# Optimization experiments

Hardware: AMD Instinct MI355X
Metric: run time of the kernel (lower is better)

## Reference

```python
import jax, jax.numpy as jnp
import numpy as np

SHIFT = 1
EPS = 1e-5

def setup_inputs() -> dict:
    key = jax.random.key(0)
    k1, k2, k3, k4, k5, k6 = jax.random.split(key, 6)
    B, C, H, Wd = 64, 512, 28, 28
    Cout = 512
    return {
        "x": jax.random.normal(k1, (B, C, H, Wd), dtype=jnp.float32),
        "W": jax.random.normal(k2, (Cout, C), dtype=jnp.float32) * 0.05,
        "gamma": jax.random.uniform(k3, (Cout,), dtype=jnp.float32) + 0.5,
        "beta": jax.random.normal(k4, (Cout,), dtype=jnp.float32) * 0.1,
        "running_mean": jax.random.normal(k5, (Cout,), dtype=jnp.float32) * 0.1,
        "running_var": jax.random.uniform(k6, (Cout,), dtype=jnp.float32) + 0.5,
    }

def reference(x, W, gamma, beta, running_mean, running_var):
    # Group-wise spatial shift: split channels into 4 groups, roll each.
    Cg = x.shape[1] // 4
    x1 = jnp.roll(x[:, 0*Cg:1*Cg], -SHIFT, axis=2)  # up
    x2 = jnp.roll(x[:, 1*Cg:2*Cg],  SHIFT, axis=2)  # down
    x3 = jnp.roll(x[:, 2*Cg:3*Cg], -SHIFT, axis=3)  # left
    x4 = jnp.roll(x[:, 3*Cg:4*Cg],  SHIFT, axis=3)  # right
    shifted = jnp.concatenate([x1, x2, x3, x4], axis=1)  # [B,C,H,W]
    # 1x1 conv (no bias) == channel matmul
    y = jnp.einsum('bchw,oc->bohw', shifted, W)
    # BatchNorm (inference: running stats) folded to scale/shift, then ReLU
    scale = gamma * jax.lax.rsqrt(running_var + EPS)
    shift = beta - running_mean * scale
    y = y * scale[None, :, None, None] + shift[None, :, None, None]
    return jnp.maximum(y, 0.0)
```

## Files before the change

kernel.cpp:

```cpp
#include <hip/hip_runtime.h>
#include <hip/hip_bf16.h>

#define BN   64
#define CIN  512
#define COUT 512
#define HW   784
#define NT   128
#define MT   112
#define BK   64
#define SW_STRIDE 72
#define SX_STRIDE 64

typedef __attribute__((ext_vector_type(8))) short short8;
typedef __attribute__((ext_vector_type(4))) float f32x4;

__device__ __forceinline__ unsigned short f2bf(float f) {
    union { float f; unsigned int u; } v; v.f = f;
    unsigned int r = v.u + 0x7fffu + ((v.u >> 16) & 1u);
    return (unsigned short)(r >> 16);
}

__device__ __forceinline__ uint2 pack4(float a, float b, float c, float d) {
    uint2 r;
    r.x = (unsigned int)f2bf(a) | ((unsigned int)f2bf(b) << 16);
    r.y = (unsigned int)f2bf(c) | ((unsigned int)f2bf(d) << 16);
    return r;
}

__global__ void wconv_kernel(const float* __restrict__ W, unsigned short* __restrict__ Wb) {
    int i = (blockIdx.x * 256 + threadIdx.x) * 8;
    float4 a = *(const float4*)(W + i);
    float4 b = *(const float4*)(W + i + 4);
    uint2 lo = pack4(a.x, a.y, a.z, a.w);
    uint2 hi = pack4(b.x, b.y, b.z, b.w);
    uint4 v; v.x = lo.x; v.y = lo.y; v.z = hi.x; v.w = hi.y;
    *(uint4*)(Wb + i) = v;
}

template<bool PREW>
__global__ __launch_bounds__(256, 2)
void shiftconv_kernel(const float* __restrict__ x,
                      const void* __restrict__ Wp,
                      const float* __restrict__ gamma,
                      const float* __restrict__ beta,
                      const float* __restrict__ rmean,
                      const float* __restrict__ rvar,
                      float* __restrict__ out)
{
    __shared__ unsigned short sW[NT * SW_STRIDE];
    __shared__ unsigned short sX[MT * SX_STRIDE];

    const int t = threadIdx.x;
    const int ot = blockIdx.x;
    const int mt = blockIdx.y;
    const int b  = blockIdx.z;
    const int o_base  = ot * NT;
    const int hw_base = mt * MT;
    const float* xb = x + (size_t)b * CIN * HW;

    const int lane = t & 63;
    const int wv   = t >> 6;
    const int m16  = lane & 15;
    const int q    = lane >> 4;

    f32x4 acc[2][7];
    #pragma unroll
    for (int i = 0; i < 2; ++i)
        #pragma unroll
        for (int j = 0; j < 7; ++j)
            acc[i][j] = (f32x4){0.f, 0.f, 0.f, 0.f};

    #pragma unroll
    for (int kk = 0; kk < CIN / BK; ++kk) {
        const int k0 = kk * BK;
        const int g  = k0 >> 7;

        #pragma unroll
        for (int e0 = 0; e0 < 2; ++e0) {
            int e = t + e0 * 256;
            if (e < (BK / 4) * (MT / 4)) {
                int cq = e / 28;
                int mq = e - cq * 28;
                int hw = hw_base + mq * 4;
                const float* src = xb + (size_t)(k0 + cq * 4) * HW;
                float4 v0, v1, v2, v3;
                if (g < 2) {
                    int shw = hw + (g == 0 ? 28 : HW - 28);
                    if (shw >= HW) shw -= HW;
                    v0 = *(const float4*)(src + 0 * HW + shw);
                    v1 = *(const float4*)(src + 1 * HW + shw);
                    v2 = *(const float4*)(src + 2 * HW + shw);
                    v3 = *(const float4*)(src + 3 * HW + shw);
                } else {
                    int h  = hw / 28;
                    int w0 = hw - h * 28;
                    int base = h * 28;
                    #pragma unroll
                    for (int j = 0; j < 4; ++j) {
                        const float* row = src + j * HW + base;
                        float4 a = *(const float4*)(row + w0);
                        float4 r;
                        if (g == 2) {
                            float ex = row[(w0 + 4 < 28) ? (w0 + 4) : 0];
                            r.x = a.y; r.y = a.z; r.z = a.w; r.w = ex;
                        } else {
                            float ex = row[(w0 == 0) ? 27 : (w0 - 1)];
                            r.x = ex; r.y = a.x; r.z = a.y; r.w = a.z;
                        }
                        if (j == 0) v0 = r; else if (j == 1) v1 = r;
                        else if (j == 2) v2 = r; else v3 = r;
                    }
                }
                int m0 = mq * 4;
                { int p = (cq + 5 * (m0 + 0)) & 15;
                  *(uint2*)(&sX[(m0 + 0) * SX_STRIDE + p * 4]) = pack4(v0.x, v1.x, v2.x, v3.x); }
                { int p = (cq + 5 * (m0 + 1)) & 15;
                  *(uint2*)(&sX[(m0 + 1) * SX_STRIDE + p * 4]) = pack4(v0.y, v1.y, v2.y, v3.y); }
                { int p = (cq + 5 * (m0 + 2)) & 15;
                  *(uint2*)(&sX[(m0 + 2) * SX_STRIDE + p * 4]) = pack4(v0.z, v1.z, v2.z, v3.z); }
                { int p = (cq + 5 * (m0 + 3)) & 15;
                  *(uint2*)(&sX[(m0 + 3) * SX_STRIDE + p * 4]) = pack4(v0.w, v1.w, v2.w, v3.w); }
            }
        }

        if (PREW) {
            const unsigned short* Wb = (const unsigned short*)Wp;
            #pragma unroll
            for (int i = 0; i < 4; ++i) {
                int e  = t + i * 256;
                int ol = e >> 3;
                int kg = (e & 7) * 8;
                uint4 v = *(const uint4*)(Wb + (size_t)(o_base + ol) * CIN + k0 + kg);
                *(uint4*)(&sW[ol * SW_STRIDE + kg]) = v;
            }
        } else {
            const float* Wf = (const float*)Wp;
            #pragma unroll
            for (int i = 0; i < 4; ++i) {
                int e  = t + i * 256;
                int ol = e >> 3;
                int kg = (e & 7) * 8;
                const float* wr = Wf + (size_t)(o_base + ol) * CIN + k0 + kg;
                float4 a = *(const float4*)(wr);
                float4 c = *(const float4*)(wr + 4);
                uint2 lo = pack4(a.x, a.y, a.z, a.w);
                uint2 hi = pack4(c.x, c.y, c.z, c.w);
                uint4 v; v.x = lo.x; v.y = lo.y; v.z = hi.x; v.w = hi.y;
                *(uint4*)(&sW[ol * SW_STRIDE + kg]) = v;
            }
        }

        __syncthreads();

        #pragma unroll
        for (int ks = 0; ks < BK; ks += 32) {
            short8 afrag[2];
            #pragma unroll
            for (int bo = 0; bo < 2; ++bo) {
                int row = wv * 32 + bo * 16 + m16;
                afrag[bo] = *(const short8*)(&sW[row * SW_STRIDE + ks + q * 8]);
            }
            #pragma unroll
            for (int bm = 0; bm < 7; ++bm) {
                int m  = bm * 16 + m16;
                int g0 = (ks >> 2) + 2 * q;
                int p0 = (g0 + 5 * m) & 15;
                int p1 = (g0 + 1 + 5 * m) & 15;
                uint2 lo = *(const uint2*)(&sX[m * SX_STRIDE + p0 * 4]);
                uint2 hi = *(const uint2*)(&sX[m * SX_STRIDE + p1 * 4]);
                union { uint2 u2[2]; short8 s; } fb;
                fb.u2[0] = lo; fb.u2[1] = hi;
                acc[0][bm] = __builtin_amdgcn_mfma_f32_16x16x32_bf16(afrag[0], fb.s, acc[0][bm], 0, 0, 0);
                acc[1][bm] = __builtin_amdgcn_mfma_f32_16x16x32_bf16(afrag[1], fb.s, acc[1][bm], 0, 0, 0);
            }
        }
        __syncthreads();
    }

    float scl[2][4], shf[2][4];
    #pragma unroll
    for (int bo = 0; bo < 2; ++bo)
        #pragma unroll
        for (int r = 0; r < 4; ++r) {
            int o = o_base + wv * 32 + bo * 16 + q * 4 + r;
            float sc = gamma[o] * rsqrtf(rvar[o] + 1e-5f);
            scl[bo][r] = sc;
            shf[bo][r] = beta[o] - rmean[o] * sc;
        }
    float* outb = out + (size_t)b * COUT * HW;
    #pragma unroll
    for (int bo = 0; bo < 2; ++bo) {
        #pragma unroll
        for (int r = 0; r < 4; ++r) {
            int o = o_base + wv * 32 + bo * 16 + q * 4 + r;
            float* orow = outb + (size_t)o * HW + hw_base + m16;
            #pragma unroll
            for (int bm = 0; bm < 7; ++bm) {
                float y = acc[bo][bm][r] * scl[bo][r] + shf[bo][r];
                y = fmaxf(y, 0.f);
                __builtin_nontemporal_store(y, orow + bm * 16);
            }
        }
    }
}

extern "C" void kernel_launch(void* const* d_in, const int* in_sizes, int n_in,
                              void* d_out, int out_size, void* d_ws, size_t ws_size,
                              hipStream_t stream)
{
    const float* x     = (const float*)d_in[0];
    const float* W     = (const float*)d_in[1];
    const float* gamma = (const float*)d_in[2];
    const float* beta  = (const float*)d_in[3];
    const float* rmean = (const float*)d_in[4];
    const float* rvar  = (const float*)d_in[5];
    float* out = (float*)d_out;

    dim3 grid(COUT / NT, HW / MT, BN);
    if (ws_size >= (size_t)(COUT * CIN * 2)) {
        wconv_kernel<<<COUT * CIN / (256 * 8), 256, 0, stream>>>(W, (unsigned short*)d_ws);
        shiftconv_kernel<true><<<grid, 256, 0, stream>>>(x, d_ws, gamma, beta, rmean, rvar, out);
    } else {
        shiftconv_kernel<false><<<grid, 256, 0, stream>>>(x, (const void*)W, gamma, beta, rmean, rvar, out);
    }
}
```

Baseline: 251.2 us.

## Split into shift+bf16 pre-pass and direct-to-LDS swizzled GEMM kernel

Adds a first kernel that applies the group shift and converts x to bf16 once, in a channel-blocked transposed layout in workspace, with the W conversion folded into the same launch. The GEMM kernel then copies the tiles with global_load_lds straight into XOR-swizzled shared memory. Before, each of the four output-channel blocks reloaded and reconverted the fp32 x tile. The cost is an extra bf16 intermediate (about 51 MB) written to and read back from HBM, plus a much larger workspace requirement. If the workspace is too small, it falls back to the old fused kernel.

```diff
diff --git a/kernel.cpp b/kernel.cpp
--- a/kernel.cpp
+++ b/kernel.cpp
@@ -8,8 +8,6 @@
 #define NT   128
 #define MT   112
 #define BK   64
-#define SW_STRIDE 72
-#define SX_STRIDE 64
 
 typedef __attribute__((ext_vector_type(8))) short short8;
 typedef __attribute__((ext_vector_type(4))) float f32x4;
@@ -27,37 +25,100 @@
     return r;
 }
 
-__global__ void wconv_kernel(const float* __restrict__ W, unsigned short* __restrict__ Wb) {
-    int i = (blockIdx.x * 256 + threadIdx.x) * 8;
-    float4 a = *(const float4*)(W + i);
-    float4 b = *(const float4*)(W + i + 4);
-    uint2 lo = pack4(a.x, a.y, a.z, a.w);
-    uint2 hi = pack4(b.x, b.y, b.z, b.w);
-    uint4 v; v.x = lo.x; v.y = lo.y; v.z = hi.x; v.w = hi.y;
-    *(uint4*)(Wb + i) = v;
-}
-
-template<bool PREW>
-__global__ __launch_bounds__(256, 2)
-void shiftconv_kernel(const float* __restrict__ x,
-                      const void* __restrict__ Wp,
-                      const float* __restrict__ gamma,
-                      const float* __restrict__ beta,
-                      const float* __restrict__ rmean,
-                      const float* __restrict__ rvar,
-                      float* __restrict__ out)
+__device__ __forceinline__ void gl_lds16(const unsigned short* g, unsigned short* l) {
+    __builtin_amdgcn_global_load_lds(
+        (const __attribute__((address_space(1))) unsigned int*)g,
+        (__attribute__((address_space(3))) unsigned int*)l,
+        16, 0, 0);
+}
+
+__global__ __launch_bounds__(256)
+void p1_shift_cvt(const float* __restrict__ x, const float* __restrict__ W,
+                  unsigned short* __restrict__ Wb, unsigned short* __restrict__ Xt)
 {
-    __shared__ unsigned short sW[NT * SW_STRIDE];
-    __shared__ unsigned short sX[MT * SX_STRIDE];
-
     const int t = threadIdx.x;
+    if (blockIdx.z == BN) {
+        int wlin = blockIdx.x * 7 + blockIdx.y;
+        for (int gi = wlin * 256 + t; gi < (COUT * CIN) / 8; gi += 56 * 256) {
+            const float* p = W + (size_t)gi * 8;
+            float4 a = *(const float4*)p;
+            float4 c = *(const float4*)(p + 4);
+            uint2 lo = pack4(a.x, a.y, a.z, a.w);
+            uint2 hi = pack4(c.x, c.y, c.z, c.w);
+            uint4 v; v.x = lo.x; v.y = lo.y; v.z = hi.x; v.w = hi.y;
+            *(uint4*)(Wb + (size_t)gi * 8) = v;
+        }
+        return;
+    }
+    const int kk = blockIdx.x;
+    const int mt = blockIdx.y;
+    const int b  = blockIdx.z;
+    const int g  = kk >> 1;
+    const int c0 = kk * BK;
+    const int hw_base = mt * MT;
+    const float* xb = x + (size_t)b * CIN * HW;
+    unsigned short* Xb = Xt + (size_t)(b * 8 + kk) * HW * BK;
+
+    #pragma unroll
+    for (int e0 = 0; e0 < 2; ++e0) {
+        int e = t + e0 * 256;
+        if (e < (BK / 4) * (MT / 4)) {
+            int cq = e / 28;
+            int mq = e - cq * 28;
+            int hw = hw_base + mq * 4;
+            const float* src = xb + (size_t)(c0 + cq * 4) * HW;
+            float4 v0, v1, v2, v3;
+            if (g < 2) {
+                int shw = hw + (g == 0 ? 28 : HW - 28);
+                if (shw >= HW) shw -= HW;
+                v0 = *(const float4*)(src + 0 * HW + shw);
+                v1 = *(const float4*)(src + 1 * HW + shw);
+                v2 = *(const float4*)(src + 2 * HW + shw);
+                v3 = *(const float4*)(src + 3 * HW + shw);
+            } else {
+                int h  = hw / 28;
+                int w0 = hw - h * 28;
+                int base = h * 28;
+                #pragma unroll
+                for (int j = 0; j < 4; ++j) {
+                    const float* row = src + j * HW + base;
+                    float4 a = *(const float4*)(row + w0);
+                    float4 r;
+                    if (g == 2) {
+                        float ex = row[(w0 + 4 < 28) ? (w0 + 4) : 0];
+                        r.x = a.y; r.y = a.z; r.z = a.w; r.w = ex;
+                    } else {
+                        float ex = row[(w0 == 0) ? 27 : (w0 - 1)];
+                        r.x = ex; r.y = a.x; r.z = a.y; r.w = a.z;
+                    }
+                    if (j == 0) v0 = r; else if (j == 1) v1 = r;
+                    else if (j == 2) v2 = r; else v3 = r;
+                }
+            }
+            unsigned short* dst = Xb + (size_t)hw * BK + cq * 4;
+            *(uint2*)(dst + 0 * BK) = pack4(v0.x, v1.x, v2.x, v3.x);
+            *(uint2*)(dst + 1 * BK) = pack4(v0.y, v1.y, v2.y, v3.y);
+            *(uint2*)(dst + 2 * BK) = pack4(v0.z, v1.z, v2.z, v3.z);
+            *(uint2*)(dst + 3 * BK) = pack4(v0.w, v1.w, v2.w, v3.w);
+        }
+    }
+}
+
+__global__ __launch_bounds__(256)
+void p2_gemm(const unsigned short* __restrict__ Wb, const unsigned short* __restrict__ Xt,
+             const float* __restrict__ gamma, const float* __restrict__ beta,
+             const float* __restrict__ rmean, const float* __restrict__ rvar,
+             float* __restrict__ out)
+{
+    __shared__ unsigned short sW[NT * BK];
+    __shared__ unsigned short sX[MT * BK];
+
+    const int t  = threadIdx.x;
     const int ot = blockIdx.x;
     const int mt = blockIdx.y;
     const int b  = blockIdx.z;
     const int o_base  = ot * NT;
     const int hw_base = mt * MT;
-    const float* xb = x + (size_t)b * CIN * HW;
-
     const int lane = t & 63;
     const int wv   = t >> 6;
     const int m16  = lane & 15;
@@ -73,14 +134,102 @@
     #pragma unroll
     for (int kk = 0; kk < CIN / BK; ++kk) {
         const int k0 = kk * BK;
-        const int g  = k0 >> 7;
-
+        const unsigned short* Wk = Wb + (size_t)o_base * CIN + k0;
+        #pragma unroll
+        for (int i = 0; i < 4; ++i) {
+            int ci = wv * 4 + i;
+            int ch = ci * 64 + lane;
+            int ol = ch >> 3, sl = ch & 7;
+            int cs = sl ^ (ol & 7);
+            gl_lds16(Wk + (size_t)ol * CIN + cs * 8, &sW[ci * 512]);
+        }
+        const unsigned short* Xk = Xt + ((size_t)(b * 8 + kk) * HW + hw_base) * BK;
+        int nci = (wv < 2) ? 4 : 3;
+        for (int i = 0; i < nci; ++i) {
+            int ci = wv + 4 * i;
+            int ch = ci * 64 + lane;
+            int hl = ch >> 3, sl = ch & 7;
+            int cs = sl ^ (hl & 7);
+            gl_lds16(Xk + hl * BK + cs * 8, &sX[ci * 512]);
+        }
+        __syncthreads();
+
+        #pragma unroll
+        for (int ks = 0; ks < BK; ks += 32) {
+            const int csb = (ks >> 3) + q;
+            short8 af[2];
+            #pragma unroll
+            for (int bo = 0; bo < 2; ++bo) {
+                int ro = wv * 32 + bo * 16 + m16;
+                af[bo] = *(const short8*)(&sW[ro * BK + (csb ^ (ro & 7)) * 8]);
+            }
+            #pragma unroll
+            for (int bm = 0; bm < 7; ++bm) {
+                int m = bm * 16 + m16;
+                short8 bf = *(const short8*)(&sX[m * BK + (csb ^ (m & 7)) * 8]);
+                acc[0][bm] = __builtin_amdgcn_mfma_f32_16x16x32_bf16(af[0], bf, acc[0][bm], 0, 0, 0);
+                acc[1][bm] = __builtin_amdgcn_mfma_f32_16x16x32_bf16(af[1], bf, acc[1][bm], 0, 0, 0);
+            }
+        }
+        __syncthreads();
+    }
+
+    float scl[2][4], shf[2][4];
+    #pragma unroll
+    for (int bo = 0; bo < 2; ++bo)
+        #pragma unroll
+        for (int r = 0; r < 4; ++r) {
+            int o = o_base + wv * 32 + bo * 16 + q * 4 + r;
+            float sc = gamma[o] * rsqrtf(rvar[o] + 1e-5f);
+            scl[bo][r] = sc;
+            shf[bo][r] = beta[o] - rmean[o] * sc;
+        }
+    float* outb = out + (size_t)b * COUT * HW;
+    #pragma unroll
+    for (int bo = 0; bo < 2; ++bo) {
+        #pragma unroll
+        for (int r = 0; r < 4; ++r) {
+            int o = o_base + wv * 32 + bo * 16 + q * 4 + r;
+            float* orow = outb + (size_t)o * HW + hw_base + m16;
+            #pragma unroll
+            for (int bm = 0; bm < 7; ++bm) {
+                float y = acc[bo][bm][r] * scl[bo][r] + shf[bo][r];
+                y = fmaxf(y, 0.f);
+                __builtin_nontemporal_store(y, orow + bm * 16);
+            }
+        }
+    }
+}
+
+#define SW_STRIDE 72
+#define SX_STRIDE 64
+__global__ __launch_bounds__(256, 2)
+void shiftconv_fallback(const float* __restrict__ x, const float* __restrict__ Wf,
+                        const float* __restrict__ gamma, const float* __restrict__ beta,
+                        const float* __restrict__ rmean, const float* __restrict__ rvar,
+                        float* __restrict__ out)
+{
+    __shared__ unsigned short sW[NT * SW_STRIDE];
+    __shared__ unsigned short sX[MT * SX_STRIDE];
+    const int t = threadIdx.x;
+    const int ot = blockIdx.x, mt = blockIdx.y, b = blockIdx.z;
+    const int o_base = ot * NT, hw_base = mt * MT;
+    const float* xb = x + (size_t)b * CIN * HW;
+    const int lane = t & 63, wv = t >> 6, m16 = lane & 15, q = lane >> 4;
+    f32x4 acc[2][7];
+    #pragma unroll
+    for (int i = 0; i < 2; ++i)
+        #pragma unroll
+        for (int j = 0; j < 7; ++j) acc[i][j] = (f32x4){0.f, 0.f, 0.f, 0.f};
+    #pragma unroll
+    for (int kk = 0; kk < CIN / BK; ++kk) {
+        const int k0 = kk * BK;
+        const int g = k0 >> 7;
         #pragma unroll
         for (int e0 = 0; e0 < 2; ++e0) {
             int e = t + e0 * 256;
             if (e < (BK / 4) * (MT / 4)) {
-                int cq = e / 28;
-                int mq = e - cq * 28;
+                int cq = e / 28, mq = e - cq * 28;
                 int hw = hw_base + mq * 4;
                 const float* src = xb + (size_t)(k0 + cq * 4) * HW;
                 float4 v0, v1, v2, v3;
@@ -92,9 +241,7 @@
                     v2 = *(const float4*)(src + 2 * HW + shw);
                     v3 = *(const float4*)(src + 3 * HW + shw);
                 } else {
-                    int h  = hw / 28;
-                    int w0 = hw - h * 28;
-                    int base = h * 28;
+                    int h = hw / 28, w0 = hw - h * 28, base = h * 28;
                     #pragma unroll
                     for (int j = 0; j < 4; ++j) {
                         const float* row = src + j * HW + base;
@@ -122,36 +269,19 @@
                   *(uint2*)(&sX[(m0 + 3) * SX_STRIDE + p * 4]) = pack4(v0.w, v1.w, v2.w, v3.w); }
             }
         }
-
-        if (PREW) {
-            const unsigned short* Wb = (const unsigned short*)Wp;
-            #pragma unroll
-            for (int i = 0; i < 4; ++i) {
-                int e  = t + i * 256;
-                int ol = e >> 3;
-                int kg = (e & 7) * 8;
-                uint4 v = *(const uint4*)(Wb + (size_t)(o_base + ol) * CIN + k0 + kg);
-                *(uint4*)(&sW[ol * SW_STRIDE + kg]) = v;
-            }
-        } else {
-            const float* Wf = (const float*)Wp;
-            #pragma unroll
-            for (int i = 0; i < 4; ++i) {
-                int e  = t + i * 256;
-                int ol = e >> 3;
-                int kg = (e & 7) * 8;
-                const float* wr = Wf + (size_t)(o_base + ol) * CIN + k0 + kg;
-                float4 a = *(const float4*)(wr);
-                float4 c = *(const float4*)(wr + 4);
-                uint2 lo = pack4(a.x, a.y, a.z, a.w);
-                uint2 hi = pack4(c.x, c.y, c.z, c.w);
-                uint4 v; v.x = lo.x; v.y = lo.y; v.z = hi.x; v.w = hi.y;
-                *(uint4*)(&sW[ol * SW_STRIDE + kg]) = v;
-            }
-        }
-
+        #pragma unroll
+        for (int i = 0; i < 4; ++i) {
+            int e = t + i * 256;
+            int ol = e >> 3, kg = (e & 7) * 8;
+            const float* wr = Wf + (size_t)(o_base + ol) * CIN + k0 + kg;
+            float4 a = *(const float4*)(wr);
+            float4 c = *(const float4*)(wr + 4);
+            uint2 lo = pack4(a.x, a.y, a.z, a.w);
+            uint2 hi = pack4(c.x, c.y, c.z, c.w);
+            uint4 v; v.x = lo.x; v.y = lo.y; v.z = hi.x; v.w = hi.y;
+            *(uint4*)(&sW[ol * SW_STRIDE + kg]) = v;
+        }
         __syncthreads();
-
         #pragma unroll
         for (int ks = 0; ks < BK; ks += 32) {
             short8 afrag[2];
@@ -162,7 +292,7 @@
             }
             #pragma unroll
             for (int bm = 0; bm < 7; ++bm) {
-                int m  = bm * 16 + m16;
+                int m = bm * 16 + m16;
                 int g0 = (ks >> 2) + 2 * q;
                 int p0 = (g0 + 5 * m) & 15;
                 int p1 = (g0 + 1 + 5 * m) & 15;
@@ -176,7 +306,6 @@
         }
         __syncthreads();
     }
-
     float scl[2][4], shf[2][4];
     #pragma unroll
     for (int bo = 0; bo < 2; ++bo)
@@ -189,7 +318,7 @@
         }
     float* outb = out + (size_t)b * COUT * HW;
     #pragma unroll
-    for (int bo = 0; bo < 2; ++bo) {
+    for (int bo = 0; bo < 2; ++bo)
         #pragma unroll
         for (int r = 0; r < 4; ++r) {
             int o = o_base + wv * 32 + bo * 16 + q * 4 + r;
@@ -201,7 +330,6 @@
                 __builtin_nontemporal_store(y, orow + bm * 16);
             }
         }
-    }
 }
 
 extern "C" void kernel_launch(void* const* d_in, const int* in_sizes, int n_in,
@@ -216,11 +344,17 @@
     const float* rvar  = (const float*)d_in[5];
     float* out = (float*)d_out;
 
-    dim3 grid(COUT / NT, HW / MT, BN);
-    if (ws_size >= (size_t)(COUT * CIN * 2)) {
-        wconv_kernel<<<COUT * CIN / (256 * 8), 256, 0, stream>>>(W, (unsigned short*)d_ws);
-        shiftconv_kernel<true><<<grid, 256, 0, stream>>>(x, d_ws, gamma, beta, rmean, rvar, out);
+    const size_t wb_bytes = (size_t)COUT * CIN * 2;
+    const size_t xt_bytes = (size_t)BN * CIN * HW * 2;
+    if (ws_size >= wb_bytes + xt_bytes) {
+        unsigned short* Wb = (unsigned short*)d_ws;
+        unsigned short* Xt = (unsigned short*)((char*)d_ws + wb_bytes);
+        dim3 g1(8, 7, BN + 1);
+        p1_shift_cvt<<<g1, 256, 0, stream>>>(x, W, Wb, Xt);
+        dim3 g2(COUT / NT, HW / MT, BN);
+        p2_gemm<<<g2, 256, 0, stream>>>(Wb, Xt, gamma, beta, rmean, rvar, out);
     } else {
-        shiftconv_kernel<false><<<grid, 256, 0, stream>>>(x, (const void*)W, gamma, beta, rmean, rvar, out);
-    }
-}
+        dim3 grid(COUT / NT, HW / MT, BN);
+        shiftconv_fallback<<<grid, 256, 0, stream>>>(x, W, gamma, beta, rmean, rvar, out);
+    }
+}
```

Result: slower. 256.3 us (+2.0%).
